# Kernel tuning notes

Hardware: AMD Instinct MI355X
Metric: run time of the kernel (lower is better)

The kernel has to match this reference:

```python
import jax, jax.numpy as jnp
import numpy as np

OBS_DIM, ACT_DIM, K, H1, H2, B = 128, 32, 16, 1024, 1024, 4096


def _init_linear(key, shape, fan_in):
    # torch nn.Linear-style uniform init U(-1/sqrt(fan_in), 1/sqrt(fan_in))
    bound = 1.0 / np.sqrt(fan_in)
    return jax.random.uniform(key, shape, jnp.float32, -bound, bound)


def setup_inputs() -> dict:
    key = jax.random.key(0)
    ks = jax.random.split(key, 9)
    in1 = OBS_DIM + ACT_DIM
    return {
        "obs": jax.random.normal(ks[0], (B, OBS_DIM), jnp.float32),
        "actions": jax.random.normal(ks[1], (B, ACT_DIM), jnp.float32),
        "comp_weights": jax.random.uniform(ks[2], (B, K), jnp.float32),
        "W1": _init_linear(ks[3], (K, in1, H1), in1),
        "b1": _init_linear(ks[4], (K, H1), in1),
        "W2": _init_linear(ks[5], (K, H1, H2), H1),
        "b2": _init_linear(ks[6], (K, H2), H1),
        "Wo": _init_linear(ks[7], (H2, 1), H2),
        "bo": _init_linear(ks[8], (1,), H2),
    }


def _comp_fc(x, cw, W, b, activate=True):
    # per-parameter-set projection: [B, K, out]
    y = jnp.einsum("bi,kio->bko", x, W) + b[None, :, :]
    # soft composition over K param sets: [B, out]
    y = jnp.einsum("bko,bk->bo", y, cw)
    return jax.nn.relu(y) if activate else y


def reference(obs, actions, comp_weights, W1, b1, W2, b2, Wo, bo):
    x = jnp.concatenate([obs, actions], axis=-1)  # [B, obs+act]
    x = _comp_fc(x, comp_weights, W1, b1)
    x = _comp_fc(x, comp_weights, W2, b2)
    return x @ Wo + bo  # [B, 1]
```

## Files before the change

### kernel.cpp

```cpp
#include <hip/hip_runtime.h>

typedef unsigned short u16;
typedef unsigned int   u32;
typedef __bf16 bf16x8 __attribute__((ext_vector_type(8)));
typedef float  f32x4  __attribute__((ext_vector_type(4)));

#define BSZ   4096
#define NK    16
#define IN1   160
#define H1D   1024
#define H2D   1024
#define K1MAIN 2560
#define K1P    2624
#define K2P    16384

__device__ __forceinline__ u16 f2bf(float f) {
    __bf16 h = (__bf16)f;
    return __builtin_bit_cast(u16, h);
}
__device__ __forceinline__ u32 pack2bf(float lo, float hi) {
    return (u32)f2bf(lo) | ((u32)f2bf(hi) << 16);
}

__device__ __forceinline__ void gload16(const void* g, void* l) {
    __builtin_amdgcn_global_load_lds(
        (const __attribute__((address_space(1))) unsigned int*)g,
        (__attribute__((address_space(3))) unsigned int*)l, 16, 0, 0);
}

__global__ void transpose_conv_kernel(const float* __restrict__ W,
                                      const float* __restrict__ bias,
                                      u16* __restrict__ outw,
                                      int Kdim, int KP)
{
    __shared__ float lt[64][65];
    const int k0 = blockIdx.x * 64, n0 = blockIdx.y * 64;
    const int c = threadIdx.x & 63, r0 = threadIdx.x >> 6;
#pragma unroll
    for (int rr = 0; rr < 16; ++rr) {
        const int r = r0 + rr * 4;
        const int kap = k0 + r;
        float v = 0.0f;
        if (kap < Kdim)            v = W[(size_t)kap * 1024 + n0 + c];
        else if (kap < Kdim + NK)  v = bias[(size_t)(kap - Kdim) * 1024 + n0 + c];
        lt[r][c] = v;
    }
    __syncthreads();
#pragma unroll
    for (int it = 0; it < 2; ++it) {
        const int q = it * 256 + threadIdx.x;
        const int nl = q >> 3, kc = q & 7;
        uint4 o;
        o.x = pack2bf(lt[kc * 8 + 0][nl], lt[kc * 8 + 1][nl]);
        o.y = pack2bf(lt[kc * 8 + 2][nl], lt[kc * 8 + 3][nl]);
        o.z = pack2bf(lt[kc * 8 + 4][nl], lt[kc * 8 + 5][nl]);
        o.w = pack2bf(lt[kc * 8 + 6][nl], lt[kc * 8 + 7][nl]);
        *reinterpret_cast<uint4*>(&outw[(size_t)(n0 + nl) * KP + k0 + kc * 8]) = o;
    }
}

__global__ __launch_bounds__(256, 2)
void gemm1_kernel(const float* __restrict__ obs,
                  const float* __restrict__ act,
                  const float* __restrict__ cw,
                  const u16* __restrict__ Bt,
                  u16* __restrict__ H1)
{
    __shared__ u16 lA[2][128 * 64];
    __shared__ u16 lB[2][64 * 64];

    const int tid = threadIdx.x;
    const int wv = tid >> 6, lane = tid & 63;
    const int l15 = lane & 15, lg = lane >> 4;
    const int bid = blockIdx.x;
    const int ntile = bid & 15, mtile = bid >> 4;
    const int brow = mtile * 128, bcol = ntile * 64;
    const int wr = (wv >> 1) * 64, wc = (wv & 1) * 32;

    f32x4 acc[4][2];
#pragma unroll
    for (int i = 0; i < 4; ++i)
#pragma unroll
        for (int j = 0; j < 2; ++j) acc[i][j] = (f32x4){0.f, 0.f, 0.f, 0.f};

    auto stageA = [&](int kt, int buf) {
#pragma unroll
        for (int it = 0; it < 4; ++it) {
            const int c = it * 256 + tid;
            const int row = c >> 3, kb = (c & 7) << 4;
            const int lkb = kb ^ ((row & 7) << 4);
            const int b_ = brow + row;
            uint4 dat;
            const int kap = kt * 64 + (lkb >> 1);
            if (kap < K1MAIN) {
                const int k = kap / IN1;
                const int i = kap - k * IN1;
                const float s = cw[b_ * NK + k];
                const float* src = (i < 128) ? (obs + (size_t)b_ * 128 + i)
                                             : (act + (size_t)b_ * 32 + (i - 128));
                float4 f0 = *reinterpret_cast<const float4*>(src);
                float4 f1 = *reinterpret_cast<const float4*>(src + 4);
                dat.x = pack2bf(f0.x * s, f0.y * s);
                dat.y = pack2bf(f0.z * s, f0.w * s);
                dat.z = pack2bf(f1.x * s, f1.y * s);
                dat.w = pack2bf(f1.z * s, f1.w * s);
            } else {
                const int base = kap - K1MAIN;
                u16 v[8];
#pragma unroll
                for (int e = 0; e < 8; ++e) {
                    const int kk2 = base + e;
                    v[e] = (kk2 < NK) ? f2bf(cw[b_ * NK + kk2]) : (u16)0;
                }
                dat.x = (u32)v[0] | ((u32)v[1] << 16);
                dat.y = (u32)v[2] | ((u32)v[3] << 16);
                dat.z = (u32)v[4] | ((u32)v[5] << 16);
                dat.w = (u32)v[6] | ((u32)v[7] << 16);
            }
            *reinterpret_cast<uint4*>(&lA[buf][row * 64 + (kb >> 1)]) = dat;
        }
    };
    auto stageB = [&](int kt, int buf) {
#pragma unroll
        for (int it = 0; it < 2; ++it) {
            const int c = it * 256 + tid;
            const int row = c >> 3, kb = (c & 7) << 4;
            const int kbS = kb ^ ((row & 7) << 4);
            gload16(Bt + (size_t)(bcol + row) * K1P + kt * 64 + (kbS >> 1),
                    &lB[buf][(it * 256 + (wv << 6)) * 8]);
        }
    };

    const int ksteps = K1P / 64;
    stageA(0, 0);
    stageB(0, 0);
    __syncthreads();
    int cur = 0;
    for (int kt = 0; kt < ksteps; ++kt) {
        if (kt + 1 < ksteps) { stageB(kt + 1, cur ^ 1); stageA(kt + 1, cur ^ 1); }
#pragma unroll
        for (int kk = 0; kk < 2; ++kk) {
            bf16x8 af[4];
            bf16x8 bfr[2];
            const int kbyte = (kk << 6) | (lg << 4);
#pragma unroll
            for (int mi = 0; mi < 4; ++mi) {
                const int r = wr + mi * 16 + l15;
                const int sl = kbyte ^ ((r & 7) << 4);
                af[mi] = *reinterpret_cast<const bf16x8*>(&lA[cur][r * 64 + (sl >> 1)]);
            }
#pragma unroll
            for (int ni = 0; ni < 2; ++ni) {
                const int r = wc + ni * 16 + l15;
                const int sl = kbyte ^ ((r & 7) << 4);
                bfr[ni] = *reinterpret_cast<const bf16x8*>(&lB[cur][r * 64 + (sl >> 1)]);
            }
#pragma unroll
            for (int mi = 0; mi < 4; ++mi)
#pragma unroll
                for (int ni = 0; ni < 2; ++ni)
                    acc[mi][ni] = __builtin_amdgcn_mfma_f32_16x16x32_bf16(
                        af[mi], bfr[ni], acc[mi][ni], 0, 0, 0);
        }
        __syncthreads();
        cur ^= 1;
    }
#pragma unroll
    for (int mi = 0; mi < 4; ++mi)
#pragma unroll
        for (int ni = 0; ni < 2; ++ni)
#pragma unroll
            for (int r = 0; r < 4; ++r) {
                float v = fmaxf(acc[mi][ni][r], 0.0f);
                const int gm = brow + wr + mi * 16 + lg * 4 + r;
                const int gn = bcol + wc + ni * 16 + l15;
                H1[(size_t)gm * 1024 + gn] = f2bf(v);
            }
}

__global__ __launch_bounds__(256, 2)
void gemm2_kernel(const u16* __restrict__ h1,
                  const float* __restrict__ cw,
                  const float* __restrict__ b2,
                  const u16* __restrict__ Bt,
                  float* __restrict__ H2a,
                  float* __restrict__ H2b)
{
    __shared__ u16 lA[2][128 * 64];
    __shared__ u16 lB[2][128 * 64];

    const int tid = threadIdx.x;
    const int wv = tid >> 6, lane = tid & 63;
    const int l15 = lane & 15, lg = lane >> 4;
    const int bid = blockIdx.x;
    const int kc = bid >> 8;
    const int r8 = bid & 255;
    const int ntile = r8 & 7, mtile = r8 >> 3;
    const int brow = mtile * 128, bcol = ntile * 128;
    const int wr = (wv >> 1) * 64, wc = (wv & 1) * 64;
    const size_t kbase = (size_t)kc * 8192;

    f32x4 part[4][4], master[4][4];
#pragma unroll
    for (int i = 0; i < 4; ++i)
#pragma unroll
        for (int j = 0; j < 4; ++j) {
            part[i][j] = (f32x4){0.f, 0.f, 0.f, 0.f};
            master[i][j] = (f32x4){0.f, 0.f, 0.f, 0.f};
        }

    auto stageA = [&](int kt, int buf) {
        const int j0 = (kt & 15) * 64;
#pragma unroll
        for (int it = 0; it < 4; ++it) {
            const int c = it * 256 + tid;
            const int row = c >> 3, kb = (c & 7) << 4;
            const int kbS = kb ^ ((row & 7) << 4);
            gload16(h1 + (size_t)(brow + row) * 1024 + j0 + (kbS >> 1),
                    &lA[buf][(it * 256 + (wv << 6)) * 8]);
        }
    };
    auto stageB = [&](int kt, int buf) {
#pragma unroll
        for (int it = 0; it < 4; ++it) {
            const int c = it * 256 + tid;
            const int row = c >> 3, kb = (c & 7) << 4;
            const int kbS = kb ^ ((row & 7) << 4);
            gload16(Bt + (size_t)(bcol + row) * K2P + kbase + kt * 64 + (kbS >> 1),
                    &lB[buf][(it * 256 + (wv << 6)) * 8]);
        }
    };

    float cwv[4][4];
    float b2v[4];

    const int ksteps = 128;
    stageB(0, 0);
    stageA(0, 0);
    __syncthreads();
    int cur = 0;
    for (int kt = 0; kt < ksteps; ++kt) {
        if (kt + 1 < ksteps) { stageB(kt + 1, cur ^ 1); stageA(kt + 1, cur ^ 1); }
        if ((kt & 15) == 0) {
            const int kg = kc * 8 + (kt >> 4);
#pragma unroll
            for (int mi = 0; mi < 4; ++mi)
#pragma unroll
                for (int r = 0; r < 4; ++r)
                    cwv[mi][r] = cw[(brow + wr + mi * 16 + lg * 4 + r) * NK + kg];
#pragma unroll
            for (int ni = 0; ni < 4; ++ni)
                b2v[ni] = b2[kg * 1024 + bcol + wc + ni * 16 + l15];
        }
#pragma unroll
        for (int kk = 0; kk < 2; ++kk) {
            bf16x8 af[4];
            bf16x8 bfr[4];
            const int kbyte = (kk << 6) | (lg << 4);
#pragma unroll
            for (int mi = 0; mi < 4; ++mi) {
                const int r = wr + mi * 16 + l15;
                const int sl = kbyte ^ ((r & 7) << 4);
                af[mi] = *reinterpret_cast<const bf16x8*>(&lA[cur][r * 64 + (sl >> 1)]);
            }
#pragma unroll
            for (int ni = 0; ni < 4; ++ni) {
                const int r = wc + ni * 16 + l15;
                const int sl = kbyte ^ ((r & 7) << 4);
                bfr[ni] = *reinterpret_cast<const bf16x8*>(&lB[cur][r * 64 + (sl >> 1)]);
            }
#pragma unroll
            for (int mi = 0; mi < 4; ++mi)
#pragma unroll
                for (int ni = 0; ni < 4; ++ni)
                    part[mi][ni] = __builtin_amdgcn_mfma_f32_16x16x32_bf16(
                        af[mi], bfr[ni], part[mi][ni], 0, 0, 0);
        }
        if ((kt & 15) == 15) {
#pragma unroll
            for (int mi = 0; mi < 4; ++mi)
#pragma unroll
                for (int ni = 0; ni < 4; ++ni)
#pragma unroll
                    for (int r = 0; r < 4; ++r) {
                        master[mi][ni][r] += cwv[mi][r] * (part[mi][ni][r] + b2v[ni]);
                        part[mi][ni][r] = 0.0f;
                    }
        }
        __syncthreads();
        cur ^= 1;
    }
    float* __restrict__ dst = kc ? H2b : H2a;
#pragma unroll
    for (int mi = 0; mi < 4; ++mi)
#pragma unroll
        for (int ni = 0; ni < 4; ++ni)
#pragma unroll
            for (int r = 0; r < 4; ++r) {
                const int gm = brow + wr + mi * 16 + lg * 4 + r;
                const int gn = bcol + wc + ni * 16 + l15;
                dst[(size_t)gm * 1024 + gn] = master[mi][ni][r];
            }
}

__global__ void gemv_out_kernel(const float* __restrict__ h2a,
                                const float* __restrict__ h2b,
                                const float* __restrict__ Wo,
                                const float* __restrict__ bo,
                                float* __restrict__ out)
{
    const int wv = threadIdx.x >> 6, lane = threadIdx.x & 63;
    const int row = blockIdx.x * 4 + wv;
    const float* ha = h2a + (size_t)row * 1024;
    const float* hb = h2b + (size_t)row * 1024;
    float s = 0.0f;
#pragma unroll
    for (int i = 0; i < 4; ++i) {
        float4 a = *reinterpret_cast<const float4*>(ha + lane * 4 + i * 256);
        float4 b = *reinterpret_cast<const float4*>(hb + lane * 4 + i * 256);
        float4 w = *reinterpret_cast<const float4*>(Wo + lane * 4 + i * 256);
        s += fmaxf(a.x + b.x, 0.f) * w.x + fmaxf(a.y + b.y, 0.f) * w.y
           + fmaxf(a.z + b.z, 0.f) * w.z + fmaxf(a.w + b.w, 0.f) * w.w;
    }
#pragma unroll
    for (int off = 32; off; off >>= 1) s += __shfl_xor(s, off, 64);
    if (lane == 0) out[row] = s + bo[0];
}

extern "C" void kernel_launch(void* const* d_in, const int* in_sizes, int n_in,
                              void* d_out, int out_size, void* d_ws, size_t ws_size,
                              hipStream_t stream)
{
    const float* obs = (const float*)d_in[0];
    const float* act = (const float*)d_in[1];
    const float* cw  = (const float*)d_in[2];
    const float* W1  = (const float*)d_in[3];
    const float* b1  = (const float*)d_in[4];
    const float* W2  = (const float*)d_in[5];
    const float* b2  = (const float*)d_in[6];
    const float* Wo  = (const float*)d_in[7];
    const float* bo  = (const float*)d_in[8];

    char* ws = (char*)d_ws;
    u16* W1T  = (u16*)ws;
    u16* W2T  = W1T + (size_t)H1D * K1P;
    u16* H1   = W2T + (size_t)H2D * K2P;
    float* H2a = (float*)(H1 + (size_t)BSZ * H1D);
    float* H2b = H2a + (size_t)BSZ * H2D;

    transpose_conv_kernel<<<dim3(K1P / 64, 16), 256, 0, stream>>>(W1, b1, W1T, K1MAIN, K1P);
    transpose_conv_kernel<<<dim3(K2P / 64, 16), 256, 0, stream>>>(W2, b2, W2T, K2P, K2P);

    gemm1_kernel<<<512, 256, 0, stream>>>(obs, act, cw, W1T, H1);
    gemm2_kernel<<<512, 256, 0, stream>>>(H1, cw, b2, W2T, H2a, H2b);

    gemv_out_kernel<<<BSZ / 4, 256, 0, stream>>>(H2a, H2b, Wo, bo, (float*)d_out);
}
```

Measured before the change: 357.0 us.

## Use 128x128 tiles with split-K in gemm1 and add combine kernel

gemm1 moves from 128x64 tiles over the full K to 128x128 tiles with a two-way split-K (41 k-steps divided into 21 and 20). Each half writes fp32 partial sums, and a new combine kernel adds them, applies ReLU and converts to bf16. The aim is more MFMA work per LDS load and better B-tile reuse while keeping 512 blocks. The cost is extra fp32 partial-sum traffic plus one more kernel launch, and the partial buffers are reused as gemm2's output scratch.

```diff
diff --git a/kernel.cpp b/kernel.cpp
--- a/kernel.cpp
+++ b/kernel.cpp
@@ -21,6 +21,8 @@
 __device__ __forceinline__ u32 pack2bf(float lo, float hi) {
     return (u32)f2bf(lo) | ((u32)f2bf(hi) << 16);
 }
+__device__ __forceinline__ float bflo(u32 u) { return __uint_as_float(u << 16); }
+__device__ __forceinline__ float bfhi(u32 u) { return __uint_as_float(u & 0xFFFF0000u); }
 
 __device__ __forceinline__ void gload16(const void* g, void* l) {
     __builtin_amdgcn_global_load_lds(
@@ -64,24 +66,26 @@
                   const float* __restrict__ act,
                   const float* __restrict__ cw,
                   const u16* __restrict__ Bt,
-                  u16* __restrict__ H1)
+                  float* __restrict__ P0,
+                  float* __restrict__ P1)
 {
     __shared__ u16 lA[2][128 * 64];
-    __shared__ u16 lB[2][64 * 64];
+    __shared__ u16 lB[2][128 * 64];
 
     const int tid = threadIdx.x;
     const int wv = tid >> 6, lane = tid & 63;
     const int l15 = lane & 15, lg = lane >> 4;
     const int bid = blockIdx.x;
-    const int ntile = bid & 15, mtile = bid >> 4;
-    const int brow = mtile * 128, bcol = ntile * 64;
-    const int wr = (wv >> 1) * 64, wc = (wv & 1) * 32;
-
-    f32x4 acc[4][2];
+    const int ntile = bid & 7, mtile = (bid >> 3) & 31, kc = bid >> 8;
+    const int brow = mtile * 128, bcol = ntile * 128;
+    const int wr = (wv >> 1) * 64, wc = (wv & 1) * 64;
+    const int kt0 = kc ? 21 : 0, ktN = kc ? 41 : 21;
+
+    f32x4 acc[4][4];
 #pragma unroll
     for (int i = 0; i < 4; ++i)
 #pragma unroll
-        for (int j = 0; j < 2; ++j) acc[i][j] = (f32x4){0.f, 0.f, 0.f, 0.f};
+        for (int j = 0; j < 4; ++j) acc[i][j] = (f32x4){0.f, 0.f, 0.f, 0.f};
 
     auto stageA = [&](int kt, int buf) {
 #pragma unroll
@@ -122,7 +126,7 @@
     };
     auto stageB = [&](int kt, int buf) {
 #pragma unroll
-        for (int it = 0; it < 2; ++it) {
+        for (int it = 0; it < 4; ++it) {
             const int c = it * 256 + tid;
             const int row = c >> 3, kb = (c & 7) << 4;
             const int kbS = kb ^ ((row & 7) << 4);
@@ -131,17 +135,16 @@
         }
     };
 
-    const int ksteps = K1P / 64;
-    stageA(0, 0);
-    stageB(0, 0);
+    stageA(kt0, 0);
+    stageB(kt0, 0);
     __syncthreads();
     int cur = 0;
-    for (int kt = 0; kt < ksteps; ++kt) {
-        if (kt + 1 < ksteps) { stageB(kt + 1, cur ^ 1); stageA(kt + 1, cur ^ 1); }
+    for (int kt = kt0; kt < ktN; ++kt) {
+        if (kt + 1 < ktN) { stageB(kt + 1, cur ^ 1); stageA(kt + 1, cur ^ 1); }
 #pragma unroll
         for (int kk = 0; kk < 2; ++kk) {
             bf16x8 af[4];
-            bf16x8 bfr[2];
+            bf16x8 bfr[4];
             const int kbyte = (kk << 6) | (lg << 4);
 #pragma unroll
             for (int mi = 0; mi < 4; ++mi) {
@@ -150,7 +153,7 @@
                 af[mi] = *reinterpret_cast<const bf16x8*>(&lA[cur][r * 64 + (sl >> 1)]);
             }
 #pragma unroll
-            for (int ni = 0; ni < 2; ++ni) {
+            for (int ni = 0; ni < 4; ++ni) {
                 const int r = wc + ni * 16 + l15;
                 const int sl = kbyte ^ ((r & 7) << 4);
                 bfr[ni] = *reinterpret_cast<const bf16x8*>(&lB[cur][r * 64 + (sl >> 1)]);
@@ -158,24 +161,41 @@
 #pragma unroll
             for (int mi = 0; mi < 4; ++mi)
 #pragma unroll
-                for (int ni = 0; ni < 2; ++ni)
+                for (int ni = 0; ni < 4; ++ni)
                     acc[mi][ni] = __builtin_amdgcn_mfma_f32_16x16x32_bf16(
                         af[mi], bfr[ni], acc[mi][ni], 0, 0, 0);
         }
         __syncthreads();
         cur ^= 1;
     }
+    float* __restrict__ dst = kc ? P1 : P0;
 #pragma unroll
     for (int mi = 0; mi < 4; ++mi)
 #pragma unroll
-        for (int ni = 0; ni < 2; ++ni)
+        for (int ni = 0; ni < 4; ++ni)
 #pragma unroll
             for (int r = 0; r < 4; ++r) {
-                float v = fmaxf(acc[mi][ni][r], 0.0f);
                 const int gm = brow + wr + mi * 16 + lg * 4 + r;
                 const int gn = bcol + wc + ni * 16 + l15;
-                H1[(size_t)gm * 1024 + gn] = f2bf(v);
-            }
+                dst[(size_t)gm * 1024 + gn] = acc[mi][ni][r];
+            }
+}
+
+__global__ void combine_h1_kernel(const float* __restrict__ P0,
+                                  const float* __restrict__ P1,
+                                  u16* __restrict__ H1)
+{
+    const size_t base = ((size_t)blockIdx.x * 256 + threadIdx.x) * 8;
+    float4 a0 = *reinterpret_cast<const float4*>(P0 + base);
+    float4 a1 = *reinterpret_cast<const float4*>(P0 + base + 4);
+    float4 b0 = *reinterpret_cast<const float4*>(P1 + base);
+    float4 b1 = *reinterpret_cast<const float4*>(P1 + base + 4);
+    uint4 o;
+    o.x = pack2bf(fmaxf(a0.x + b0.x, 0.f), fmaxf(a0.y + b0.y, 0.f));
+    o.y = pack2bf(fmaxf(a0.z + b0.z, 0.f), fmaxf(a0.w + b0.w, 0.f));
+    o.z = pack2bf(fmaxf(a1.x + b1.x, 0.f), fmaxf(a1.y + b1.y, 0.f));
+    o.w = pack2bf(fmaxf(a1.z + b1.z, 0.f), fmaxf(a1.w + b1.w, 0.f));
+    *reinterpret_cast<uint4*>(&H1[base]) = o;
 }
 
 __global__ __launch_bounds__(256, 2)
@@ -345,14 +365,16 @@
     u16* W1T  = (u16*)ws;
     u16* W2T  = W1T + (size_t)H1D * K1P;
     u16* H1   = W2T + (size_t)H2D * K2P;
-    float* H2a = (float*)(H1 + (size_t)BSZ * H1D);
-    float* H2b = H2a + (size_t)BSZ * H2D;
+    float* Pa = (float*)(H1 + (size_t)BSZ * H1D);
+    float* Pb = Pa + (size_t)BSZ * H2D;
 
     transpose_conv_kernel<<<dim3(K1P / 64, 16), 256, 0, stream>>>(W1, b1, W1T, K1MAIN, K1P);
     transpose_conv_kernel<<<dim3(K2P / 64, 16), 256, 0, stream>>>(W2, b2, W2T, K2P, K2P);
 
-    gemm1_kernel<<<512, 256, 0, stream>>>(obs, act, cw, W1T, H1);
-    gemm2_kernel<<<512, 256, 0, stream>>>(H1, cw, b2, W2T, H2a, H2b);
-
-    gemv_out_kernel<<<BSZ / 4, 256, 0, stream>>>(H2a, H2b, Wo, bo, (float*)d_out);
-}
+    gemm1_kernel<<<512, 256, 0, stream>>>(obs, act, cw, W1T, Pa, Pb);
+    combine_h1_kernel<<<BSZ * H1D / (256 * 8), 256, 0, stream>>>(Pa, Pb, H1);
+
+    gemm2_kernel<<<512, 256, 0, stream>>>(H1, cw, b2, W2T, Pa, Pb);
+
+    gemv_out_kernel<<<BSZ / 4, 256, 0, stream>>>(Pa, Pb, Wo, bo, (float*)d_out);
+}
```

After: 346.9 us. 1.03x faster.
